# Performance work log

Hardware: AMD Instinct MI355X
Metric: run time of the kernel (lower is better)

The kernel has to match this reference:

```python
import jax, jax.numpy as jnp
import numpy as np

B, T = 512, 2048
IN1, H1, H2 = 1, 64, 16


def _lstm_params(key, in_dim, hid):
    k = 1.0 / np.sqrt(hid)
    ks = jax.random.split(key, 4)
    u = lambda kk, shape: jax.random.uniform(kk, shape, jnp.float32, -k, k)
    return (u(ks[0], (4 * hid, in_dim)),  # w_ih, PyTorch gate order i,f,g,o
            u(ks[1], (4 * hid, hid)),     # w_hh
            u(ks[2], (4 * hid,)),         # b_ih
            u(ks[3], (4 * hid,)))         # b_hh


def setup_inputs() -> dict:
    key = jax.random.key(0)
    kx, k1, k2 = jax.random.split(key, 3)
    x = jax.random.normal(kx, (B, T, IN1), dtype=jnp.float32)
    w_ih1, w_hh1, b_ih1, b_hh1 = _lstm_params(k1, IN1, H1)
    w_ih2, w_hh2, b_ih2, b_hh2 = _lstm_params(k2, H1, H2)
    return {"x": x,
            "w_ih1": w_ih1, "w_hh1": w_hh1, "b_ih1": b_ih1, "b_hh1": b_hh1,
            "w_ih2": w_ih2, "w_hh2": w_hh2, "b_ih2": b_ih2, "b_hh2": b_hh2}


def _lstm(x, w_ih, w_hh, b_ih, b_hh):
    # x: [B, T, in]; returns all hidden states [B, T, H]
    hid = w_hh.shape[1]
    # precompute input contribution for every timestep: [T, B, 4H]
    xg = jnp.einsum('bti,gi->tbg', x, w_ih) + b_ih + b_hh
    h0 = jnp.zeros((x.shape[0], hid), x.dtype)
    c0 = jnp.zeros((x.shape[0], hid), x.dtype)

    def step(carry, xt):
        h, c = carry
        gates = xt + h @ w_hh.T                       # [B, 4H]
        i, f, g, o = jnp.split(gates, 4, axis=-1)     # PyTorch order
        i = jax.nn.sigmoid(i)
        f = jax.nn.sigmoid(f)
        g = jnp.tanh(g)
        o = jax.nn.sigmoid(o)
        c = f * c + i * g
        h = o * jnp.tanh(c)
        return (h, c), h

    _, hs = jax.lax.scan(step, (h0, c0), xg)          # hs: [T, B, H]
    return jnp.transpose(hs, (1, 0, 2))               # [B, T, H]


def reference(x, w_ih1, w_hh1, b_ih1, b_hh1, w_ih2, w_hh2, b_ih2, b_hh2):
    h1 = _lstm(x, w_ih1, w_hh1, b_ih1, b_hh1)   # [B, T, 64]
    h2 = _lstm(h1, w_ih2, w_hh2, b_ih2, b_hh2)  # [B, T, 16]
    return h2
```

## Files before the change

### kernel.cpp

```cpp
#include <hip/hip_runtime.h>

#define TSTEPS 2048
#define NBATCH 512
#define H1 64
#define H2 16

typedef _Float16 h2v __attribute__((ext_vector_type(2)));

__device__ __forceinline__ float fsig(float x) {
    return __builtin_amdgcn_rcpf(1.0f + __builtin_amdgcn_exp2f(-1.4426950408889634f * x));
}
__device__ __forceinline__ float ftanh(float x) {
    return 1.0f - 2.0f * __builtin_amdgcn_rcpf(1.0f + __builtin_amdgcn_exp2f(2.8853900817779268f * x));
}
__device__ __forceinline__ float act(float x, float k2) {
    return k2 * fsig(k2 * x) - (k2 - 1.0f);
}

#if __has_builtin(__builtin_amdgcn_fdot2)
__device__ __forceinline__ float dot2(int wp, int hp, float acc) {
    return __builtin_amdgcn_fdot2(__builtin_bit_cast(h2v, wp),
                                  __builtin_bit_cast(h2v, hp), acc, false);
}
#else
__device__ __forceinline__ float dot2(int wp, int hp, float acc) {
    h2v a = __builtin_bit_cast(h2v, wp), b = __builtin_bit_cast(h2v, hp);
    return acc + (float)a.x * (float)b.x + (float)a.y * (float)b.y;
}
#endif

__device__ __forceinline__ int packh2(float a, float b) {
    h2v v; v.x = (_Float16)a; v.y = (_Float16)b;
    return __builtin_bit_cast(int, v);
}
template<int CTRL>
__device__ __forceinline__ float dpp_bcast(float v) {
    int r = __builtin_amdgcn_mov_dpp(__float_as_int(v), CTRL, 0xF, 0xF, true);
    return __int_as_float(r);
}

__global__ void __launch_bounds__(64, 1)
__attribute__((amdgpu_waves_per_eu(1, 1)))
lstm2_fused(const float* __restrict__ x,
            const float* __restrict__ w_ih1,
            const float* __restrict__ w_hh1,
            const float* __restrict__ b_ih1,
            const float* __restrict__ b_hh1,
            const float* __restrict__ w_ih2,
            const float* __restrict__ w_hh2,
            const float* __restrict__ b_ih2,
            const float* __restrict__ b_hh2,
            float* __restrict__ out)
{
    const int lane = threadIdx.x;
    const int b    = blockIdx.x;

    __shared__ int4     wlds[26][64];
    __shared__ float    x_lds[TSTEPS];
    __shared__ _Float16 h1_lds[H1];
    __shared__ _Float16 h2_lds[H2];
    __shared__ float    ring[32][H2];

    {
        const float4* xs = (const float4*)(x + (size_t)b * TSTEPS);
        float4* xd = (float4*)x_lds;
        #pragma unroll
        for (int i = 0; i < 8; ++i) xd[lane + 64 * i] = xs[lane + 64 * i];
    }
    if (lane < 32) ((int*)h1_lds)[lane] = 0;
    if (lane < 8)  ((int*)h2_lds)[lane] = 0;

    int w1i[32], w1f[32];
    {
        const float* wri = w_hh1 + (size_t)lane * H1;
        const float* wrf = w_hh1 + (size_t)(H1 + lane) * H1;
        #pragma unroll
        for (int k = 0; k < 32; ++k) {
            w1i[k] = packh2(wri[2 * k], wri[2 * k + 1]);
            w1f[k] = packh2(wrf[2 * k], wrf[2 * k + 1]);
        }
    }
    const int m  = lane >> 2;
    const int g2 = lane & 3;
    const int r2 = g2 * H2 + m;
    {
        const float* wrg = w_hh1 + (size_t)(2 * H1 + lane) * H1;
        const float* wro = w_hh1 + (size_t)(3 * H1 + lane) * H1;
        const float* wr2 = w_ih2 + (size_t)r2 * H1;
        #pragma unroll
        for (int tq = 0; tq < 8; ++tq) {
            wlds[tq][lane] = make_int4(
                packh2(wrg[8*tq+0], wrg[8*tq+1]), packh2(wrg[8*tq+2], wrg[8*tq+3]),
                packh2(wrg[8*tq+4], wrg[8*tq+5]), packh2(wrg[8*tq+6], wrg[8*tq+7]));
            wlds[8 + tq][lane] = make_int4(
                packh2(wro[8*tq+0], wro[8*tq+1]), packh2(wro[8*tq+2], wro[8*tq+3]),
                packh2(wro[8*tq+4], wro[8*tq+5]), packh2(wro[8*tq+6], wro[8*tq+7]));
            wlds[16 + tq][lane] = make_int4(
                packh2(wr2[8*tq+0], wr2[8*tq+1]), packh2(wr2[8*tq+2], wr2[8*tq+3]),
                packh2(wr2[8*tq+4], wr2[8*tq+5]), packh2(wr2[8*tq+6], wr2[8*tq+7]));
        }
        const float* wrh = w_hh2 + (size_t)r2 * H2;
        wlds[24][lane] = make_int4(packh2(wrh[0], wrh[1]),  packh2(wrh[2], wrh[3]),
                                   packh2(wrh[4], wrh[5]),  packh2(wrh[6], wrh[7]));
        wlds[25][lane] = make_int4(packh2(wrh[8], wrh[9]),  packh2(wrh[10], wrh[11]),
                                   packh2(wrh[12], wrh[13]), packh2(wrh[14], wrh[15]));
    }

    const float wxi = w_ih1[lane],        wxf = w_ih1[H1 + lane];
    const float wxg = w_ih1[2*H1 + lane], wxo = w_ih1[3*H1 + lane];
    const float bsi = b_ih1[lane] + b_hh1[lane];
    const float bsf = b_ih1[H1+lane] + b_hh1[H1+lane];
    const float bsg = b_ih1[2*H1+lane] + b_hh1[2*H1+lane];
    const float bso = b_ih1[3*H1+lane] + b_hh1[3*H1+lane];
    const float bs2 = b_ih2[r2] + b_hh2[r2];
    const float k22 = (g2 == 2) ? 2.0f : 1.0f;

    float c1 = 0.0f;
    float c2 = 0.0f;
    float* outb = out + (size_t)b * TSTEPS * H2;

    const int4* wl = &wlds[0][0];

    for (int p = 0; p <= TSTEPS; ++p) {
        const int tau_f = p - 1;
        if (tau_f >= 31 && (tau_f & 15) == 15) {
            const int tau0 = (tau_f & ~15) - 16;
            const int tt = tau0 + (lane >> 2), ch0 = (lane & 3) * 4;
            float4 v = *(const float4*)&ring[tt & 31][ch0];
            *(float4*)(outb + (size_t)tt * H2 + ch0) = v;
        }

        const float xv = x_lds[p & (TSTEPS - 1)];
        float ai = bsi + wxi * xv;
        float af = bsf + wxf * xv;
        float ag = bsg + wxg * xv;
        float ao = bso + wxo * xv;
        float a0 = bs2, a1 = 0.f, a2a = 0.f, a3 = 0.f;
        int4 vh0, vh1;

        {
            const int4* hs4 = (const int4*)h1_lds;
            #pragma unroll
            for (int c = 0; c < 4; ++c) {
                int4 hA = hs4[2*c], hB = hs4[2*c + 1];
                int4 cg  = wl[(2*c)      * 64 + lane];
                int4 cg2 = wl[(2*c + 1)  * 64 + lane];
                int4 co  = wl[(8 + 2*c)  * 64 + lane];
                int4 co2 = wl[(9 + 2*c)  * 64 + lane];
                int4 cu  = wl[(16 + 2*c) * 64 + lane];
                int4 cu2 = wl[(17 + 2*c) * 64 + lane];
                if (c == 2) { vh0 = wl[24 * 64 + lane]; vh1 = wl[25 * 64 + lane]; }

                ai = dot2(w1i[8*c+0], hA.x, ai); ai = dot2(w1i[8*c+1], hA.y, ai);
                ai = dot2(w1i[8*c+2], hA.z, ai); ai = dot2(w1i[8*c+3], hA.w, ai);
                ai = dot2(w1i[8*c+4], hB.x, ai); ai = dot2(w1i[8*c+5], hB.y, ai);
                ai = dot2(w1i[8*c+6], hB.z, ai); ai = dot2(w1i[8*c+7], hB.w, ai);

                af = dot2(w1f[8*c+0], hA.x, af); af = dot2(w1f[8*c+1], hA.y, af);
                af = dot2(w1f[8*c+2], hA.z, af); af = dot2(w1f[8*c+3], hA.w, af);
                af = dot2(w1f[8*c+4], hB.x, af); af = dot2(w1f[8*c+5], hB.y, af);
                af = dot2(w1f[8*c+6], hB.z, af); af = dot2(w1f[8*c+7], hB.w, af);

                ag = dot2(cg.x,  hA.x, ag); ag = dot2(cg.y,  hA.y, ag);
                ag = dot2(cg.z,  hA.z, ag); ag = dot2(cg.w,  hA.w, ag);
                ag = dot2(cg2.x, hB.x, ag); ag = dot2(cg2.y, hB.y, ag);
                ag = dot2(cg2.z, hB.z, ag); ag = dot2(cg2.w, hB.w, ag);

                ao = dot2(co.x,  hA.x, ao); ao = dot2(co.y,  hA.y, ao);
                ao = dot2(co.z,  hA.z, ao); ao = dot2(co.w,  hA.w, ao);
                ao = dot2(co2.x, hB.x, ao); ao = dot2(co2.y, hB.y, ao);
                ao = dot2(co2.z, hB.z, ao); ao = dot2(co2.w, hB.w, ao);

                a0  = dot2(cu.x,  hA.x, a0);  a1  = dot2(cu.y,  hA.y, a1);
                a2a = dot2(cu.z,  hA.z, a2a); a3  = dot2(cu.w,  hA.w, a3);
                a0  = dot2(cu2.x, hB.x, a0);  a1  = dot2(cu2.y, hB.y, a1);
                a2a = dot2(cu2.z, hB.z, a2a); a3  = dot2(cu2.w, hB.w, a3);
            }
        }

        if (p < TSTEPS) {
            float gi = fsig(ai), gf = fsig(af), gg = ftanh(ag), go = fsig(ao);
            c1 = gf * c1 + gi * gg;
            float h1n = go * ftanh(c1);
            h1_lds[lane] = (_Float16)h1n;
        }

        if (p >= 1) {
            const int4* hs = (const int4*)h2_lds;
            int4 u0 = hs[0], u1 = hs[1];
            a0  = dot2(vh0.x, u0.x, a0);  a1  = dot2(vh0.y, u0.y, a1);
            a2a = dot2(vh0.z, u0.z, a2a); a3  = dot2(vh0.w, u0.w, a3);
            a0  = dot2(vh1.x, u1.x, a0);  a1  = dot2(vh1.y, u1.y, a1);
            a2a = dot2(vh1.z, u1.z, a2a); a3  = dot2(vh1.w, u1.w, a3);
            float av = act((a0 + a1) + (a2a + a3), k22);
            float gi = dpp_bcast<0x00>(av);
            float gf = dpp_bcast<0x55>(av);
            float gg = dpp_bcast<0xAA>(av);
            float go = dpp_bcast<0xFF>(av);
            c2 = gf * c2 + gi * gg;
            float h2n = go * ftanh(c2);
            if (g2 == 0) {
                h2_lds[m] = (_Float16)h2n;
                ring[(p - 1) & 31][m] = h2n;
            }
        }
    }

    {
        const int tt = 2032 + (lane >> 2), ch0 = (lane & 3) * 4;
        float4 v = *(const float4*)&ring[tt & 31][ch0];
        *(float4*)(outb + (size_t)tt * H2 + ch0) = v;
    }
}

extern "C" void kernel_launch(void* const* d_in, const int* in_sizes, int n_in,
                              void* d_out, int out_size, void* d_ws, size_t ws_size,
                              hipStream_t stream) {
    const float* x     = (const float*)d_in[0];
    const float* w_ih1 = (const float*)d_in[1];
    const float* w_hh1 = (const float*)d_in[2];
    const float* b_ih1 = (const float*)d_in[3];
    const float* b_hh1 = (const float*)d_in[4];
    const float* w_ih2 = (const float*)d_in[5];
    const float* w_hh2 = (const float*)d_in[6];
    const float* b_ih2 = (const float*)d_in[7];
    const float* b_hh2 = (const float*)d_in[8];
    float* out = (float*)d_out;

    lstm2_fused<<<NBATCH, 64, 0, stream>>>(x, w_ih1, w_hh1, b_ih1, b_hh1,
                                           w_ih2, w_hh2, b_ih2, b_hh2, out);
}
```

Baseline: 1.170 ms.

## Keep recurrent weights in AGPRs instead of LDS and prefetch hidden state

Moves the g/o gate weights of layer 1 and the layer-2 input weights out of LDS into accumulation registers, read each step with v_accvgpr_read, and keeps the layer-2 recurrent weights in VGPRs. It also software-pipelines the h1 LDS reads one chunk ahead and hoists the h2 read to the top of the step. The aim is to cut per-step LDS traffic and latency on the serial recurrence. The cost is many extra accvgpr moves per step and volatile asm that may limit scheduling; a stale read of h1 at the step boundary relies on LDS ordering within a single wave.

```diff
diff --git a/kernel.cpp b/kernel.cpp
--- a/kernel.cpp
+++ b/kernel.cpp
@@ -38,6 +38,9 @@
     int r = __builtin_amdgcn_mov_dpp(__float_as_int(v), CTRL, 0xF, 0xF, true);
     return __int_as_float(r);
 }
+
+#define AWRITE(dst, src) asm volatile("v_accvgpr_write_b32 %0, %1" : "=a"(dst) : "v"(src))
+#define AREAD(dst, src)  asm volatile("v_accvgpr_read_b32 %0, %1"  : "=v"(dst) : "a"(src))
 
 __global__ void __launch_bounds__(64, 1)
 __attribute__((amdgpu_waves_per_eu(1, 1)))
@@ -55,7 +58,6 @@
     const int lane = threadIdx.x;
     const int b    = blockIdx.x;
 
-    __shared__ int4     wlds[26][64];
     __shared__ float    x_lds[TSTEPS];
     __shared__ _Float16 h1_lds[H1];
     __shared__ _Float16 h2_lds[H2];
@@ -80,30 +82,30 @@
             w1f[k] = packh2(wrf[2 * k], wrf[2 * k + 1]);
         }
     }
+
     const int m  = lane >> 2;
     const int g2 = lane & 3;
     const int r2 = g2 * H2 + m;
+    int ag_g[32], ag_o[32], ag_u[32];
     {
         const float* wrg = w_hh1 + (size_t)(2 * H1 + lane) * H1;
         const float* wro = w_hh1 + (size_t)(3 * H1 + lane) * H1;
         const float* wr2 = w_ih2 + (size_t)r2 * H1;
         #pragma unroll
-        for (int tq = 0; tq < 8; ++tq) {
-            wlds[tq][lane] = make_int4(
-                packh2(wrg[8*tq+0], wrg[8*tq+1]), packh2(wrg[8*tq+2], wrg[8*tq+3]),
-                packh2(wrg[8*tq+4], wrg[8*tq+5]), packh2(wrg[8*tq+6], wrg[8*tq+7]));
-            wlds[8 + tq][lane] = make_int4(
-                packh2(wro[8*tq+0], wro[8*tq+1]), packh2(wro[8*tq+2], wro[8*tq+3]),
-                packh2(wro[8*tq+4], wro[8*tq+5]), packh2(wro[8*tq+6], wro[8*tq+7]));
-            wlds[16 + tq][lane] = make_int4(
-                packh2(wr2[8*tq+0], wr2[8*tq+1]), packh2(wr2[8*tq+2], wr2[8*tq+3]),
-                packh2(wr2[8*tq+4], wr2[8*tq+5]), packh2(wr2[8*tq+6], wr2[8*tq+7]));
-        }
+        for (int k = 0; k < 32; ++k) {
+            int vg = packh2(wrg[2 * k], wrg[2 * k + 1]);
+            int vo = packh2(wro[2 * k], wro[2 * k + 1]);
+            int vu = packh2(wr2[2 * k], wr2[2 * k + 1]);
+            AWRITE(ag_g[k], vg);
+            AWRITE(ag_o[k], vo);
+            AWRITE(ag_u[k], vu);
+        }
+    }
+    int wh2r[8];
+    {
         const float* wrh = w_hh2 + (size_t)r2 * H2;
-        wlds[24][lane] = make_int4(packh2(wrh[0], wrh[1]),  packh2(wrh[2], wrh[3]),
-                                   packh2(wrh[4], wrh[5]),  packh2(wrh[6], wrh[7]));
-        wlds[25][lane] = make_int4(packh2(wrh[8], wrh[9]),  packh2(wrh[10], wrh[11]),
-                                   packh2(wrh[12], wrh[13]), packh2(wrh[14], wrh[15]));
+        #pragma unroll
+        for (int k = 0; k < 8; ++k) wh2r[k] = packh2(wrh[2 * k], wrh[2 * k + 1]);
     }
 
     const float wxi = w_ih1[lane],        wxf = w_ih1[H1 + lane];
@@ -119,9 +121,13 @@
     float c2 = 0.0f;
     float* outb = out + (size_t)b * TSTEPS * H2;
 
-    const int4* wl = &wlds[0][0];
+    const int4* hs4 = (const int4*)h1_lds;
+    int4 hA = make_int4(0, 0, 0, 0), hB = make_int4(0, 0, 0, 0);
 
     for (int p = 0; p <= TSTEPS; ++p) {
+        const int4* h2p = (const int4*)h2_lds;
+        int4 u0 = h2p[0], u1 = h2p[1];
+
         const int tau_f = p - 1;
         if (tau_f >= 31 && (tau_f & 15) == 15) {
             const int tau0 = (tau_f & ~15) - 16;
@@ -131,67 +137,65 @@
         }
 
         const float xv = x_lds[p & (TSTEPS - 1)];
-        float ai = bsi + wxi * xv;
-        float af = bsf + wxf * xv;
-        float ag = bsg + wxg * xv;
-        float ao = bso + wxo * xv;
+        float aI = bsi + wxi * xv;
+        float aF = bsf + wxf * xv;
+        float aG = bsg + wxg * xv;
+        float aO = bso + wxo * xv;
         float a0 = bs2, a1 = 0.f, a2a = 0.f, a3 = 0.f;
-        int4 vh0, vh1;
-
-        {
-            const int4* hs4 = (const int4*)h1_lds;
+
+        #pragma unroll
+        for (int c = 0; c < 4; ++c) {
+            int wg[8], wo[8], wu[8];
             #pragma unroll
-            for (int c = 0; c < 4; ++c) {
-                int4 hA = hs4[2*c], hB = hs4[2*c + 1];
-                int4 cg  = wl[(2*c)      * 64 + lane];
-                int4 cg2 = wl[(2*c + 1)  * 64 + lane];
-                int4 co  = wl[(8 + 2*c)  * 64 + lane];
-                int4 co2 = wl[(9 + 2*c)  * 64 + lane];
-                int4 cu  = wl[(16 + 2*c) * 64 + lane];
-                int4 cu2 = wl[(17 + 2*c) * 64 + lane];
-                if (c == 2) { vh0 = wl[24 * 64 + lane]; vh1 = wl[25 * 64 + lane]; }
-
-                ai = dot2(w1i[8*c+0], hA.x, ai); ai = dot2(w1i[8*c+1], hA.y, ai);
-                ai = dot2(w1i[8*c+2], hA.z, ai); ai = dot2(w1i[8*c+3], hA.w, ai);
-                ai = dot2(w1i[8*c+4], hB.x, ai); ai = dot2(w1i[8*c+5], hB.y, ai);
-                ai = dot2(w1i[8*c+6], hB.z, ai); ai = dot2(w1i[8*c+7], hB.w, ai);
-
-                af = dot2(w1f[8*c+0], hA.x, af); af = dot2(w1f[8*c+1], hA.y, af);
-                af = dot2(w1f[8*c+2], hA.z, af); af = dot2(w1f[8*c+3], hA.w, af);
-                af = dot2(w1f[8*c+4], hB.x, af); af = dot2(w1f[8*c+5], hB.y, af);
-                af = dot2(w1f[8*c+6], hB.z, af); af = dot2(w1f[8*c+7], hB.w, af);
-
-                ag = dot2(cg.x,  hA.x, ag); ag = dot2(cg.y,  hA.y, ag);
-                ag = dot2(cg.z,  hA.z, ag); ag = dot2(cg.w,  hA.w, ag);
-                ag = dot2(cg2.x, hB.x, ag); ag = dot2(cg2.y, hB.y, ag);
-                ag = dot2(cg2.z, hB.z, ag); ag = dot2(cg2.w, hB.w, ag);
-
-                ao = dot2(co.x,  hA.x, ao); ao = dot2(co.y,  hA.y, ao);
-                ao = dot2(co.z,  hA.z, ao); ao = dot2(co.w,  hA.w, ao);
-                ao = dot2(co2.x, hB.x, ao); ao = dot2(co2.y, hB.y, ao);
-                ao = dot2(co2.z, hB.z, ao); ao = dot2(co2.w, hB.w, ao);
-
-                a0  = dot2(cu.x,  hA.x, a0);  a1  = dot2(cu.y,  hA.y, a1);
-                a2a = dot2(cu.z,  hA.z, a2a); a3  = dot2(cu.w,  hA.w, a3);
-                a0  = dot2(cu2.x, hB.x, a0);  a1  = dot2(cu2.y, hB.y, a1);
-                a2a = dot2(cu2.z, hB.z, a2a); a3  = dot2(cu2.w, hB.w, a3);
+            for (int j = 0; j < 8; ++j) {
+                AREAD(wg[j], ag_g[8*c + j]);
+                AREAD(wo[j], ag_o[8*c + j]);
+                AREAD(wu[j], ag_u[8*c + j]);
             }
+            int4 nA, nB;
+            if (c < 3) { nA = hs4[2*c + 2]; nB = hs4[2*c + 3]; }
+
+            aI = dot2(w1i[8*c+0], hA.x, aI); aI = dot2(w1i[8*c+1], hA.y, aI);
+            aI = dot2(w1i[8*c+2], hA.z, aI); aI = dot2(w1i[8*c+3], hA.w, aI);
+            aI = dot2(w1i[8*c+4], hB.x, aI); aI = dot2(w1i[8*c+5], hB.y, aI);
+            aI = dot2(w1i[8*c+6], hB.z, aI); aI = dot2(w1i[8*c+7], hB.w, aI);
+
+            aF = dot2(w1f[8*c+0], hA.x, aF); aF = dot2(w1f[8*c+1], hA.y, aF);
+            aF = dot2(w1f[8*c+2], hA.z, aF); aF = dot2(w1f[8*c+3], hA.w, aF);
+            aF = dot2(w1f[8*c+4], hB.x, aF); aF = dot2(w1f[8*c+5], hB.y, aF);
+            aF = dot2(w1f[8*c+6], hB.z, aF); aF = dot2(w1f[8*c+7], hB.w, aF);
+
+            aG = dot2(wg[0], hA.x, aG); aG = dot2(wg[1], hA.y, aG);
+            aG = dot2(wg[2], hA.z, aG); aG = dot2(wg[3], hA.w, aG);
+            aG = dot2(wg[4], hB.x, aG); aG = dot2(wg[5], hB.y, aG);
+            aG = dot2(wg[6], hB.z, aG); aG = dot2(wg[7], hB.w, aG);
+
+            aO = dot2(wo[0], hA.x, aO); aO = dot2(wo[1], hA.y, aO);
+            aO = dot2(wo[2], hA.z, aO); aO = dot2(wo[3], hA.w, aO);
+            aO = dot2(wo[4], hB.x, aO); aO = dot2(wo[5], hB.y, aO);
+            aO = dot2(wo[6], hB.z, aO); aO = dot2(wo[7], hB.w, aO);
+
+            a0  = dot2(wu[0], hA.x, a0);  a1  = dot2(wu[1], hA.y, a1);
+            a2a = dot2(wu[2], hA.z, a2a); a3  = dot2(wu[3], hA.w, a3);
+            a0  = dot2(wu[4], hB.x, a0);  a1  = dot2(wu[5], hB.y, a1);
+            a2a = dot2(wu[6], hB.z, a2a); a3  = dot2(wu[7], hB.w, a3);
+
+            if (c < 3) { hA = nA; hB = nB; }
         }
 
         if (p < TSTEPS) {
-            float gi = fsig(ai), gf = fsig(af), gg = ftanh(ag), go = fsig(ao);
+            float gi = fsig(aI), gf = fsig(aF), gg = ftanh(aG), go = fsig(aO);
             c1 = gf * c1 + gi * gg;
             float h1n = go * ftanh(c1);
             h1_lds[lane] = (_Float16)h1n;
         }
+        hA = hs4[0]; hB = hs4[1];
 
         if (p >= 1) {
-            const int4* hs = (const int4*)h2_lds;
-            int4 u0 = hs[0], u1 = hs[1];
-            a0  = dot2(vh0.x, u0.x, a0);  a1  = dot2(vh0.y, u0.y, a1);
-            a2a = dot2(vh0.z, u0.z, a2a); a3  = dot2(vh0.w, u0.w, a3);
-            a0  = dot2(vh1.x, u1.x, a0);  a1  = dot2(vh1.y, u1.y, a1);
-            a2a = dot2(vh1.z, u1.z, a2a); a3  = dot2(vh1.w, u1.w, a3);
+            a0  = dot2(wh2r[0], u0.x, a0);  a1  = dot2(wh2r[1], u0.y, a1);
+            a2a = dot2(wh2r[2], u0.z, a2a); a3  = dot2(wh2r[3], u0.w, a3);
+            a0  = dot2(wh2r[4], u1.x, a0);  a1  = dot2(wh2r[5], u1.y, a1);
+            a2a = dot2(wh2r[6], u1.z, a2a); a3  = dot2(wh2r[7], u1.w, a3);
             float av = act((a0 + a1) + (a2a + a3), k22);
             float gi = dpp_bcast<0x00>(av);
             float gf = dpp_bcast<0x55>(av);
```

Result: slower. 1.583 ms (+35.2%).
